# Kernel optimization log

Hardware: AMD Instinct MI355X
Metric: run time of the kernel (lower is better)

Reference implementation:

```python
import jax, jax.numpy as jnp
import numpy as np

E, H, V, B, T = 512, 512, 32000, 64, 20


def setup_inputs() -> dict:
    key = jax.random.key(0)
    ks = jax.random.split(key, 10)
    s = 0.05
    return {
        "features": jax.random.normal(ks[0], (B, E), jnp.float32),
        "captions": jax.random.randint(ks[1], (B, T), 0, V),
        "lenghts": jax.random.randint(ks[2], (B,), 1, T),
        "emb_table": jax.random.normal(ks[3], (V, E), jnp.float32) * s,
        "w_ih": jax.random.normal(ks[4], (4 * H, E), jnp.float32) * s,
        "w_hh": jax.random.normal(ks[5], (4 * H, H), jnp.float32) * s,
        "b_ih": jax.random.normal(ks[6], (4 * H,), jnp.float32) * s,
        "b_hh": jax.random.normal(ks[7], (4 * H,), jnp.float32) * s,
        "fc_w": jax.random.normal(ks[8], (V, H), jnp.float32) * s,
        "fc_b": jax.random.normal(ks[9], (V,), jnp.float32) * s,
    }


def _lstm(xs, w_ih, w_hh, b_ih, b_hh):
    # xs: [B, T+1, E] -> hidden states [B, T+1, H], PyTorch gate order i,f,g,o
    b, _, _ = xs.shape
    h0 = jnp.zeros((b, w_hh.shape[1]), xs.dtype)
    c0 = jnp.zeros_like(h0)
    bias = b_ih + b_hh

    def step(carry, x_t):
        h, c = carry
        gates = x_t @ w_ih.T + h @ w_hh.T + bias  # [B, 4H]
        i, f, g, o = jnp.split(gates, 4, axis=-1)
        i, f, o = jax.nn.sigmoid(i), jax.nn.sigmoid(f), jax.nn.sigmoid(o)
        g = jnp.tanh(g)
        c = f * c + i * g
        h = o * jnp.tanh(c)
        return (h, c), h

    _, hs = jax.lax.scan(step, (h0, c0), jnp.swapaxes(xs, 0, 1))  # hs: [T+1, B, H]
    return jnp.swapaxes(hs, 0, 1)


def reference(features, captions, lenghts, emb_table, w_ih, w_hh, b_ih, b_hh, fc_w, fc_b):
    embeddings = emb_table[captions]                       # [B, T, E]
    xs = jnp.concatenate([features[:, None, :], embeddings], axis=1)  # [B, T+1, E]
    hs = _lstm(xs, w_ih, w_hh, b_ih, b_hh)[:, 1:, :]       # [B, T, H]
    logits = hs @ fc_w.T + fc_b                            # [B, T, V]
    # original loops softmax over each 1-D vocab slice == softmax over last axis
    return jax.nn.softmax(logits, axis=-1)
```

## Files before the change

kernel.cpp:

```cpp
#include <hip/hip_runtime.h>
#include <cstdint>
#include <cstddef>

#define E_DIM 512
#define H_DIM 512
#define V_DIM 32000
#define B_DIM 64
#define T_DIM 20
#define NBLK 32
#define NBLK_TOT 256
#define PT_LDS 68
#define HS_STR 532

typedef _Float16 f16;
typedef _Float16 f16x8 __attribute__((ext_vector_type(8)));
typedef _Float16 f16x4 __attribute__((ext_vector_type(4)));
typedef float    f32x4 __attribute__((ext_vector_type(4)));

__device__ __forceinline__ void async_lds16(void* lds, const void* g) {
  __builtin_amdgcn_global_load_lds(
      (const __attribute__((address_space(1))) uint32_t*)g,
      (__attribute__((address_space(3))) uint32_t*)lds, 16, 0, 0);
}

__device__ __forceinline__ float sigmoidf_(float x) {
  return 1.0f / (1.0f + expf(-x));
}

__device__ __forceinline__ f16x8 load_h8_coh(const f16* p) {
  union { unsigned long long u[2]; f16x8 v; } r;
  r.u[0] = __hip_atomic_load((const unsigned long long*)p,
                             __ATOMIC_RELAXED, __HIP_MEMORY_SCOPE_AGENT);
  r.u[1] = __hip_atomic_load((const unsigned long long*)(p + 4),
                             __ATOMIC_RELAXED, __HIP_MEMORY_SCOPE_AGENT);
  return r.v;
}
__device__ __forceinline__ void store_h4_coh(f16* p, f16x4 v) {
  union { f16x4 h; unsigned long long u; } cvt;
  cvt.h = v;
  __hip_atomic_store((unsigned long long*)p, cvt.u,
                     __ATOMIC_RELAXED, __HIP_MEMORY_SCOPE_AGENT);
}

__global__ __launch_bounds__(128) void gather_x16_kernel(
    const float* __restrict__ features, const int* __restrict__ captions,
    const float* __restrict__ emb, f16* __restrict__ x16) {
  const int m = blockIdx.x;
  const int j = threadIdx.x;
  f16x4 r4 = {(f16)0.f, (f16)0.f, (f16)0.f, (f16)0.f};
  if (m < 1344) {
    const int b = m & 63;
    const int t = m >> 6;
    const float* src = (t == 0)
        ? features + (size_t)b * E_DIM
        : emb + (size_t)captions[b * T_DIM + (t - 1)] * E_DIM;
    const float4 v = ((const float4*)src)[j];
    r4.x = (f16)v.x; r4.y = (f16)v.y; r4.z = (f16)v.z; r4.w = (f16)v.w;
  }
  ((f16x4*)(x16 + (size_t)m * 512))[j] = r4;
}

__global__ __launch_bounds__(256) void convert_w_kernel(
    const float* __restrict__ w, f16* __restrict__ w16) {
  const int i = blockIdx.x * 256 + threadIdx.x;
  const float4 v = ((const float4*)w)[i];
  f16x4 r;
  r.x = (f16)v.x; r.y = (f16)v.y; r.z = (f16)v.z; r.w = (f16)v.w;
  ((f16x4*)w16)[i] = r;
}

__global__ __launch_bounds__(256) void bias_sum_kernel(
    const float* __restrict__ a, const float* __restrict__ b,
    float* __restrict__ o) {
  const int i = blockIdx.x * 256 + threadIdx.x;
  if (i < 2048) o[i] = a[i] + b[i];
}

__global__ __launch_bounds__(256) void gemm16_kernel(
    const f16* __restrict__ A, const f16* __restrict__ Bw,
    const float* __restrict__ bias, float* __restrict__ C, int ldc,
    int mode) {
  __shared__ f16 As[128 * 64];
  __shared__ f16 Bs[128 * 64];
  const int tid = threadIdx.x;
  const int lane = tid & 63;
  const int wid = tid >> 6;
  const int m0 = blockIdx.y * 128;
  const int n0 = blockIdx.x * 128;
  const int wm = (wid >> 1) * 64;
  const int wn = (wid & 1) * 64;

  f32x4 acc[4][4];
#pragma unroll
  for (int i = 0; i < 4; ++i)
#pragma unroll
    for (int j = 0; j < 4; ++j) {
      f32x4 z = {0.f, 0.f, 0.f, 0.f};
      acc[i][j] = z;
    }
  const int lr = lane & 15;
  const int lkb = (lane >> 4) * 8;

  for (int kt = 0; kt < 512; kt += 64) {
#pragma unroll
    for (int i = 0; i < 4; ++i) {
      const int off = i * 4096 + wid * 1024 + lane * 16;
      const int row = off >> 7;
      const int colh = (off & 127) >> 1;
      async_lds16((char*)As + i * 4096 + wid * 1024,
                  A + (size_t)(m0 + row) * 512 + kt + colh);
      async_lds16((char*)Bs + i * 4096 + wid * 1024,
                  Bw + (size_t)(n0 + row) * 512 + kt + colh);
    }
    __syncthreads();
#pragma unroll
    for (int ks = 0; ks < 2; ++ks) {
      f16x8 af[4], bf[4];
#pragma unroll
      for (int mi = 0; mi < 4; ++mi)
        af[mi] = *(const f16x8*)&As[(wm + mi * 16 + lr) * 64 + ks * 32 + lkb];
#pragma unroll
      for (int ni = 0; ni < 4; ++ni)
        bf[ni] = *(const f16x8*)&Bs[(wn + ni * 16 + lr) * 64 + ks * 32 + lkb];
#pragma unroll
      for (int mi = 0; mi < 4; ++mi)
#pragma unroll
        for (int ni = 0; ni < 4; ++ni)
          acc[mi][ni] = __builtin_amdgcn_mfma_f32_16x16x32_f16(
              af[mi], bf[ni], acc[mi][ni], 0, 0, 0);
    }
    __syncthreads();
  }

#pragma unroll
  for (int mi = 0; mi < 4; ++mi) {
    const int mbase = m0 + wm + mi * 16 + (lane >> 4) * 4;
#pragma unroll
    for (int ni = 0; ni < 4; ++ni) {
      const int n = n0 + wn + ni * 16 + lr;
      const float bv = bias[n];
#pragma unroll
      for (int r = 0; r < 4; ++r) {
        const int mr = mbase + r;
        size_t off;
        if (mode == 2)
          off = (size_t)(mr >> 6) * (2048 * 64) + (size_t)n * 64 + (mr & 63);
        else if (mode == 1)
          off = (size_t)((mr & 63) * 20 + (mr >> 6)) * ldc + n;
        else
          off = (size_t)mr * ldc + n;
        C[off] = acc[mi][ni][r] + bv;
      }
    }
  }
}

__global__ __launch_bounds__(256) void gemm16_f16out_kernel(
    const f16* __restrict__ A, const f16* __restrict__ Bw,
    const float* __restrict__ bias, f16* __restrict__ C16) {
  __shared__ f16 As[128 * 64];
  __shared__ f16 Bs[128 * 64];
  const int tid = threadIdx.x;
  const int lane = tid & 63;
  const int wid = tid >> 6;
  const int m0 = blockIdx.y * 128;
  const int n0 = blockIdx.x * 128;
  const int wm = (wid >> 1) * 64;
  const int wn = (wid & 1) * 64;

  f32x4 acc[4][4];
#pragma unroll
  for (int i = 0; i < 4; ++i)
#pragma unroll
    for (int j = 0; j < 4; ++j) {
      f32x4 z = {0.f, 0.f, 0.f, 0.f};
      acc[i][j] = z;
    }
  const int lr = lane & 15;
  const int lkb = (lane >> 4) * 8;

  for (int kt = 0; kt < 512; kt += 64) {
#pragma unroll
    for (int i = 0; i < 4; ++i) {
      const int off = i * 4096 + wid * 1024 + lane * 16;
      const int row = off >> 7;
      const int colh = (off & 127) >> 1;
      async_lds16((char*)As + i * 4096 + wid * 1024,
                  A + (size_t)(m0 + row) * 512 + kt + colh);
      async_lds16((char*)Bs + i * 4096 + wid * 1024,
                  Bw + (size_t)(n0 + row) * 512 + kt + colh);
    }
    __syncthreads();
#pragma unroll
    for (int ks = 0; ks < 2; ++ks) {
      f16x8 af[4], bf[4];
#pragma unroll
      for (int mi = 0; mi < 4; ++mi)
        af[mi] = *(const f16x8*)&As[(wm + mi * 16 + lr) * 64 + ks * 32 + lkb];
#pragma unroll
      for (int ni = 0; ni < 4; ++ni)
        bf[ni] = *(const f16x8*)&Bs[(wn + ni * 16 + lr) * 64 + ks * 32 + lkb];
#pragma unroll
      for (int mi = 0; mi < 4; ++mi)
#pragma unroll
        for (int ni = 0; ni < 4; ++ni)
          acc[mi][ni] = __builtin_amdgcn_mfma_f32_16x16x32_f16(
              af[mi], bf[ni], acc[mi][ni], 0, 0, 0);
    }
    __syncthreads();
  }

#pragma unroll
  for (int mi = 0; mi < 4; ++mi) {
    const int mbase = m0 + wm + mi * 16 + (lane >> 4) * 4;
#pragma unroll
    for (int ni = 0; ni < 4; ++ni) {
      const int n = n0 + wn + ni * 16 + lr;
      const float bv = bias[n];
#pragma unroll
      for (int r = 0; r < 4; ++r) {
        const int mr = mbase + r;
        const int orow = (mr & 63) * 20 + (mr >> 6);
        C16[(size_t)orow * 32000 + n] = (f16)(acc[mi][ni][r] + bv);
      }
    }
  }
}

__global__ __launch_bounds__(256, 1) void lstm_persistent7(
    const float* __restrict__ PT, const f16* __restrict__ Whh,
    f16* __restrict__ hsT, unsigned* __restrict__ flags,
    const float* __restrict__ fcw, f16* __restrict__ w16) {
  __shared__ f16 hS[64 * HS_STR];
  __shared__ float pT[64 * PT_LDS];
  __shared__ f16 hS2[64 * 16];
  const int tid = threadIdx.x;

  if (blockIdx.x >= NBLK) {
    const int g0 = (blockIdx.x - NBLK) * 256 + tid;
    for (int i = g0; i < 4096000; i += (NBLK_TOT - NBLK) * 256) {
      const float4 v = ((const float4*)fcw)[i];
      f16x4 r;
      r.x = (f16)v.x; r.y = (f16)v.y; r.z = (f16)v.z; r.w = (f16)v.w;
      ((f16x4*)w16)[i] = r;
    }
    return;
  }

  const int lane = tid & 63;
  const int w = tid >> 6;
  const int u0 = blockIdx.x * 16;
  const int fr = lane & 15;
  const int fq = lane >> 4;
  const int q = fr >> 2;
  const int jw = fr & 3;
  const int grow = q * 512 + u0 + w * 4 + jw;

  f16x8 bW[16];
  {
    const f16* brow = Whh + (size_t)grow * 512;
#pragma unroll
    for (int kk = 0; kk < 16; ++kk)
      bW[kk] = *(const f16x8*)&brow[kk * 32 + fq * 8];
  }

  for (int i = tid; i < 64 * 16; i += 256) {
    const int rr = i >> 4;
    const int q4 = i & 15;
    const int g = rr >> 4, ul = rr & 15;
    const float4 v =
        *(const float4*)&PT[((size_t)(g * 512 + u0 + ul)) * 64 + q4 * 4];
    *(float4*)&pT[rr * PT_LDS + q4 * 4] = v;
  }

  float cr[4] = {0.f, 0.f, 0.f, 0.f};

  for (int t = 0; t <= T_DIM; ++t) {
    if (t > 0) {
      const f16* src = hsT + (size_t)(t - 1) * (64 * 512)
                           + (size_t)(w * 16) * 512;
      f16x8 hrow[16];
#pragma unroll
      for (int j = 0; j < 16; ++j)
        hrow[j] = load_h8_coh(src + (size_t)j * 512 + lane * 8);
#pragma unroll
      for (int j = 0; j < 16; ++j)
        *(f16x8*)&hS[(w * 16 + j) * HS_STR + lane * 8] = hrow[j];
    }
    __syncthreads();

    f32x4 acc[4];
#pragma unroll
    for (int mi = 0; mi < 4; ++mi) {
      f32x4 z = {0.f, 0.f, 0.f, 0.f};
      acc[mi] = z;
    }
    if (t > 0) {
#pragma unroll
      for (int mi = 0; mi < 4; ++mi) {
        f16x8 a[16];
#pragma unroll
        for (int kk = 0; kk < 16; ++kk)
          a[kk] =
              *(const f16x8*)&hS[(mi * 16 + fr) * HS_STR + kk * 32 + fq * 8];
#pragma unroll
        for (int kk = 0; kk < 16; ++kk)
          acc[mi] = __builtin_amdgcn_mfma_f32_16x16x32_f16(a[kk], bW[kk],
                                                           acc[mi], 0, 0, 0);
      }
    }
    const int prow = (q * 16 + w * 4 + jw) * PT_LDS;
#pragma unroll
    for (int mi = 0; mi < 4; ++mi)
#pragma unroll
      for (int r = 0; r < 4; ++r)
        acc[mi][r] += pT[prow + mi * 16 + fq * 4 + r];

#pragma unroll
    for (int r = 0; r < 4; ++r) {
      const float y0 = acc[0][r], y1 = acc[1][r], y2 = acc[2][r],
                  y3 = acc[3][r];
      const float f0 = __shfl_xor(y0, 4),  f1 = __shfl_xor(y1, 4),
                  f2 = __shfl_xor(y2, 4),  f3 = __shfl_xor(y3, 4);
      const float g0 = __shfl_xor(y0, 8),  g1 = __shfl_xor(y1, 8),
                  g2 = __shfl_xor(y2, 8),  g3 = __shfl_xor(y3, 8);
      const float o0 = __shfl_xor(y0, 12), o1 = __shfl_xor(y1, 12),
                  o2 = __shfl_xor(y2, 12), o3 = __shfl_xor(y3, 12);
      const float x  = q == 0 ? y0 : q == 1 ? y1 : q == 2 ? y2 : y3;
      const float xf = q == 0 ? f0 : q == 1 ? f1 : q == 2 ? f2 : f3;
      const float xg = q == 0 ? g0 : q == 1 ? g1 : q == 2 ? g2 : g3;
      const float xo = q == 0 ? o0 : q == 1 ? o1 : q == 2 ? o2 : o3;
      const float gi = q == 0 ? x  : q == 1 ? xf : q == 2 ? xg : xo;
      const float gf = q == 0 ? xf : q == 1 ? x  : q == 2 ? xo : xg;
      const float gg = q == 0 ? xg : q == 1 ? xo : q == 2 ? x  : xf;
      const float go = q == 0 ? xo : q == 1 ? xg : q == 2 ? xf : x;
      const float si = sigmoidf_(gi);
      const float sf = sigmoidf_(gf);
      const float tg = tanhf(gg);
      const float so = sigmoidf_(go);
      const float cn = sf * cr[r] + si * tg;
      cr[r] = cn;
      const float hn = so * tanhf(cn);
      const int b = q * 16 + fq * 4 + r;
      hS2[b * 16 + w * 4 + jw] = (f16)hn;
    }
    __syncthreads();

    {
      f16* slab = hsT + (size_t)t * (64 * 512);
      const int row = tid >> 2;
      const int c4 = tid & 3;
      const f16x4 v = *(const f16x4*)&hS2[row * 16 + c4 * 4];
      store_h4_coh(slab + (size_t)row * 512 + u0 + c4 * 4, v);
    }

    if (t < T_DIM) {
      for (int i = tid; i < 64 * 16; i += 256) {
        const int rr = i >> 4;
        const int q4 = i & 15;
        const int g = rr >> 4, ul = rr & 15;
        const float4 v = *(const float4*)
            &PT[((size_t)(t + 1) * 2048 + g * 512 + u0 + ul) * 64 + q4 * 4];
        *(float4*)&pT[rr * PT_LDS + q4 * 4] = v;
      }
      asm volatile("s_waitcnt vmcnt(0)" ::: "memory");
      __syncthreads();
      if (tid == 0)
        __hip_atomic_store(&flags[blockIdx.x * 16], (unsigned)(t + 1),
                           __ATOMIC_RELAXED, __HIP_MEMORY_SCOPE_AGENT);
      if (tid < NBLK) {
        while (__hip_atomic_load(&flags[tid * 16], __ATOMIC_RELAXED,
                                 __HIP_MEMORY_SCOPE_AGENT) < (unsigned)(t + 1))
          __builtin_amdgcn_s_sleep(3);
      }
      __syncthreads();
    }
  }
}

__device__ __forceinline__ float waveMax(float v) {
#pragma unroll
  for (int o = 32; o > 0; o >>= 1) v = fmaxf(v, __shfl_down(v, o));
  return v;
}
__device__ __forceinline__ float waveSum(float v) {
#pragma unroll
  for (int o = 32; o > 0; o >>= 1) v += __shfl_down(v, o);
  return v;
}

__global__ __launch_bounds__(1024) void softmax_f16_kernel(
    const f16* __restrict__ lg, float* __restrict__ out) {
  const f16x8* L = (const f16x8*)(lg + (size_t)blockIdx.x * V_DIM);
  float4* p4 = (float4*)(out + (size_t)blockIdx.x * V_DIM);
  const int t = threadIdx.x;
  __shared__ float sred[16];

  float4 v[8];
  float m = -1e30f;
#pragma unroll
  for (int j = 0; j < 4; ++j) {
    const int i = j * 1024 + t;
    if (i < 4000) {
      const f16x8 h = L[i];
      v[2 * j].x     = (float)h[0]; v[2 * j].y     = (float)h[1];
      v[2 * j].z     = (float)h[2]; v[2 * j].w     = (float)h[3];
      v[2 * j + 1].x = (float)h[4]; v[2 * j + 1].y = (float)h[5];
      v[2 * j + 1].z = (float)h[6]; v[2 * j + 1].w = (float)h[7];
      m = fmaxf(m, fmaxf(fmaxf(v[2 * j].x, v[2 * j].y),
                         fmaxf(v[2 * j].z, v[2 * j].w)));
      m = fmaxf(m, fmaxf(fmaxf(v[2 * j + 1].x, v[2 * j + 1].y),
                         fmaxf(v[2 * j + 1].z, v[2 * j + 1].w)));
    }
  }
  m = waveMax(m);
  if ((t & 63) == 0) sred[t >> 6] = m;
  __syncthreads();
  float mb = sred[0];
#pragma unroll
  for (int k = 1; k < 16; ++k) mb = fmaxf(mb, sred[k]);
  __syncthreads();

  float s = 0.f;
#pragma unroll
  for (int j = 0; j < 8; ++j) {
    const int i = (j >> 1) * 1024 + t;
    if (i < 4000) {
      v[j].x = expf(v[j].x - mb);
      v[j].y = expf(v[j].y - mb);
      v[j].z = expf(v[j].z - mb);
      v[j].w = expf(v[j].w - mb);
      s += v[j].x + v[j].y + v[j].z + v[j].w;
    }
  }
  s = waveSum(s);
  if ((t & 63) == 0) sred[t >> 6] = s;
  __syncthreads();
  float sb = sred[0];
#pragma unroll
  for (int k = 1; k < 16; ++k) sb += sred[k];
  const float inv = 1.0f / sb;

#pragma unroll
  for (int j = 0; j < 4; ++j) {
    const int i = j * 1024 + t;
    if (i < 4000) {
      float4 a = v[2 * j], b = v[2 * j + 1];
      a.x *= inv; a.y *= inv; a.z *= inv; a.w *= inv;
      b.x *= inv; b.y *= inv; b.z *= inv; b.w *= inv;
      p4[2 * i] = a;
      p4[2 * i + 1] = b;
    }
  }
}

__global__ __launch_bounds__(1024) void softmax_reg_kernel(
    float* __restrict__ out) {
  float4* p4 = (float4*)(out + (size_t)blockIdx.x * V_DIM);
  const int t = threadIdx.x;
  __shared__ float sred[16];
  float4 v[8];
  float m = -1e30f;
#pragma unroll
  for (int j = 0; j < 8; ++j) {
    const int i = j * 1024 + t;
    if (i < 8000) {
      v[j] = p4[i];
      m = fmaxf(m, fmaxf(fmaxf(v[j].x, v[j].y), fmaxf(v[j].z, v[j].w)));
    }
  }
  m = waveMax(m);
  if ((t & 63) == 0) sred[t >> 6] = m;
  __syncthreads();
  float mb = sred[0];
#pragma unroll
  for (int k = 1; k < 16; ++k) mb = fmaxf(mb, sred[k]);
  __syncthreads();
  float s = 0.f;
#pragma unroll
  for (int j = 0; j < 8; ++j) {
    const int i = j * 1024 + t;
    if (i < 8000) {
      v[j].x = expf(v[j].x - mb);
      v[j].y = expf(v[j].y - mb);
      v[j].z = expf(v[j].z - mb);
      v[j].w = expf(v[j].w - mb);
      s += v[j].x + v[j].y + v[j].z + v[j].w;
    }
  }
  s = waveSum(s);
  if ((t & 63) == 0) sred[t >> 6] = s;
  __syncthreads();
  float sb = sred[0];
#pragma unroll
  for (int k = 1; k < 16; ++k) sb += sred[k];
  const float inv = 1.0f / sb;
#pragma unroll
  for (int j = 0; j < 8; ++j) {
    const int i = j * 1024 + t;
    if (i < 8000) {
      float4 o;
      o.x = v[j].x * inv; o.y = v[j].y * inv;
      o.z = v[j].z * inv; o.w = v[j].w * inv;
      p4[i] = o;
    }
  }
}

extern "C" void kernel_launch(void* const* d_in, const int* in_sizes, int n_in,
                              void* d_out, int out_size, void* d_ws, size_t ws_size,
                              hipStream_t stream) {
  const float* features = (const float*)d_in[0];
  const int*   captions = (const int*)d_in[1];
  const float* emb      = (const float*)d_in[3];
  const float* w_ih     = (const float*)d_in[4];
  const float* w_hh     = (const float*)d_in[5];
  const float* b_ih     = (const float*)d_in[6];
  const float* b_hh     = (const float*)d_in[7];
  const float* fc_w     = (const float*)d_in[8];
  const float* fc_b     = (const float*)d_in[9];
  float* out = (float*)d_out;

  char* ws = (char*)d_ws;
  unsigned* flags = (unsigned*)ws; ws += 2048;
  f16* hsT = (f16*)ws;  ws += (size_t)21 * B_DIM * H_DIM * 2;
  f16* w16 = (f16*)ws;  ws += (size_t)V_DIM * H_DIM * 2;
  f16* logits16 = (f16*)ws;
  const size_t ws_need_f16logits =
      ((char*)logits16 - (char*)d_ws) + (size_t)1280 * V_DIM * 2;
  const bool use_f16_logits = ws_size >= ws_need_f16logits;

  float* PT    = out;
  f16*   x16   = (f16*)(out + 3000000);
  f16*   wih16 = (f16*)(out + 3400000);
  f16*   whh16 = (f16*)(out + 4000000);
  float* bsum  = out + 4600000;

  hipMemsetAsync(flags, 0, 2048, stream);

  gather_x16_kernel<<<1408, 128, 0, stream>>>(features, captions, emb, x16);
  convert_w_kernel<<<1024, 256, 0, stream>>>(w_ih, wih16);
  convert_w_kernel<<<1024, 256, 0, stream>>>(w_hh, whh16);
  bias_sum_kernel<<<8, 256, 0, stream>>>(b_ih, b_hh, bsum);

  gemm16_kernel<<<dim3(16, 11), 256, 0, stream>>>(x16, wih16, bsum, PT, 0, 2);

  lstm_persistent7<<<NBLK_TOT, 256, 0, stream>>>(PT, whh16, hsT, flags,
                                                 fc_w, w16);

  const f16* Afc = hsT + (size_t)B_DIM * H_DIM;
  if (use_f16_logits) {
    gemm16_f16out_kernel<<<dim3(250, 10), 256, 0, stream>>>(Afc, w16, fc_b,
                                                            logits16);
    softmax_f16_kernel<<<1280, 1024, 0, stream>>>(logits16, out);
  } else {
    gemm16_kernel<<<dim3(250, 10), 256, 0, stream>>>(Afc, w16, fc_b, out,
                                                     32000, 1);
    softmax_reg_kernel<<<1280, 1024, 0, stream>>>(out);
  }
}
```

Baseline: 308.2 us.

## Fuse FC GEMM into persistent LSTM kernel with dynamic tile queue and per-timestep flags

Merges the output-projection GEMM into the persistent LSTM kernel. After the recurrence (or the fc_w conversion), blocks pull 128x128 tiles from an atomic queue. Each tile waits only on the LSTM flags for the timesteps it needs, so FC work on early timesteps can overlap the remaining recurrence and one kernel launch disappears. The cost is spin-waiting and a non-async, coherent load path for the A operand. The GEMM also runs on only 256 blocks at one block per CU, fewer than the original 2500-block grid.

Result: slower. 372.1 us (+20.7%).

```diff
diff --git a/kernel.cpp b/kernel.cpp
--- a/kernel.cpp
+++ b/kernel.cpp
@@ -11,6 +11,7 @@
 #define NBLK_TOT 256
 #define PT_LDS 68
 #define HS_STR 532
+#define N_TILES 2500
 
 typedef _Float16 f16;
 typedef _Float16 f16x8 __attribute__((ext_vector_type(8)));
@@ -155,86 +156,20 @@
   }
 }
 
-__global__ __launch_bounds__(256) void gemm16_f16out_kernel(
-    const f16* __restrict__ A, const f16* __restrict__ Bw,
-    const float* __restrict__ bias, f16* __restrict__ C16) {
-  __shared__ f16 As[128 * 64];
-  __shared__ f16 Bs[128 * 64];
-  const int tid = threadIdx.x;
-  const int lane = tid & 63;
-  const int wid = tid >> 6;
-  const int m0 = blockIdx.y * 128;
-  const int n0 = blockIdx.x * 128;
-  const int wm = (wid >> 1) * 64;
-  const int wn = (wid & 1) * 64;
-
-  f32x4 acc[4][4];
-#pragma unroll
-  for (int i = 0; i < 4; ++i)
-#pragma unroll
-    for (int j = 0; j < 4; ++j) {
-      f32x4 z = {0.f, 0.f, 0.f, 0.f};
-      acc[i][j] = z;
-    }
-  const int lr = lane & 15;
-  const int lkb = (lane >> 4) * 8;
-
-  for (int kt = 0; kt < 512; kt += 64) {
-#pragma unroll
-    for (int i = 0; i < 4; ++i) {
-      const int off = i * 4096 + wid * 1024 + lane * 16;
-      const int row = off >> 7;
-      const int colh = (off & 127) >> 1;
-      async_lds16((char*)As + i * 4096 + wid * 1024,
-                  A + (size_t)(m0 + row) * 512 + kt + colh);
-      async_lds16((char*)Bs + i * 4096 + wid * 1024,
-                  Bw + (size_t)(n0 + row) * 512 + kt + colh);
-    }
-    __syncthreads();
-#pragma unroll
-    for (int ks = 0; ks < 2; ++ks) {
-      f16x8 af[4], bf[4];
-#pragma unroll
-      for (int mi = 0; mi < 4; ++mi)
-        af[mi] = *(const f16x8*)&As[(wm + mi * 16 + lr) * 64 + ks * 32 + lkb];
-#pragma unroll
-      for (int ni = 0; ni < 4; ++ni)
-        bf[ni] = *(const f16x8*)&Bs[(wn + ni * 16 + lr) * 64 + ks * 32 + lkb];
-#pragma unroll
-      for (int mi = 0; mi < 4; ++mi)
-#pragma unroll
-        for (int ni = 0; ni < 4; ++ni)
-          acc[mi][ni] = __builtin_amdgcn_mfma_f32_16x16x32_f16(
-              af[mi], bf[ni], acc[mi][ni], 0, 0, 0);
-    }
-    __syncthreads();
-  }
-
-#pragma unroll
-  for (int mi = 0; mi < 4; ++mi) {
-    const int mbase = m0 + wm + mi * 16 + (lane >> 4) * 4;
-#pragma unroll
-    for (int ni = 0; ni < 4; ++ni) {
-      const int n = n0 + wn + ni * 16 + lr;
-      const float bv = bias[n];
-#pragma unroll
-      for (int r = 0; r < 4; ++r) {
-        const int mr = mbase + r;
-        const int orow = (mr & 63) * 20 + (mr >> 6);
-        C16[(size_t)orow * 32000 + n] = (f16)(acc[mi][ni][r] + bv);
-      }
-    }
-  }
-}
-
-__global__ __launch_bounds__(256, 1) void lstm_persistent7(
+__global__ __launch_bounds__(256, 1) void mega_kernel(
     const float* __restrict__ PT, const f16* __restrict__ Whh,
     f16* __restrict__ hsT, unsigned* __restrict__ flags,
-    const float* __restrict__ fcw, f16* __restrict__ w16) {
+    const float* __restrict__ fcw, f16* __restrict__ w16,
+    const float* __restrict__ fcb, f16* __restrict__ logits16,
+    unsigned* __restrict__ convDone, unsigned* __restrict__ queue,
+    int do_fc) {
   __shared__ f16 hS[64 * HS_STR];
   __shared__ float pT[64 * PT_LDS];
   __shared__ f16 hS2[64 * 16];
+  __shared__ unsigned tileS;
   const int tid = threadIdx.x;
+  const int lane = tid & 63;
+  const int w = tid >> 6;
 
   if (blockIdx.x >= NBLK) {
     const int g0 = (blockIdx.x - NBLK) * 256 + tid;
@@ -242,138 +177,247 @@
       const float4 v = ((const float4*)fcw)[i];
       f16x4 r;
       r.x = (f16)v.x; r.y = (f16)v.y; r.z = (f16)v.z; r.w = (f16)v.w;
-      ((f16x4*)w16)[i] = r;
-    }
-    return;
-  }
-
-  const int lane = tid & 63;
-  const int w = tid >> 6;
-  const int u0 = blockIdx.x * 16;
-  const int fr = lane & 15;
-  const int fq = lane >> 4;
-  const int q = fr >> 2;
-  const int jw = fr & 3;
-  const int grow = q * 512 + u0 + w * 4 + jw;
-
-  f16x8 bW[16];
-  {
-    const f16* brow = Whh + (size_t)grow * 512;
-#pragma unroll
-    for (int kk = 0; kk < 16; ++kk)
-      bW[kk] = *(const f16x8*)&brow[kk * 32 + fq * 8];
-  }
-
-  for (int i = tid; i < 64 * 16; i += 256) {
-    const int rr = i >> 4;
-    const int q4 = i & 15;
-    const int g = rr >> 4, ul = rr & 15;
-    const float4 v =
-        *(const float4*)&PT[((size_t)(g * 512 + u0 + ul)) * 64 + q4 * 4];
-    *(float4*)&pT[rr * PT_LDS + q4 * 4] = v;
-  }
-
-  float cr[4] = {0.f, 0.f, 0.f, 0.f};
-
-  for (int t = 0; t <= T_DIM; ++t) {
-    if (t > 0) {
-      const f16* src = hsT + (size_t)(t - 1) * (64 * 512)
-                           + (size_t)(w * 16) * 512;
-      f16x8 hrow[16];
-#pragma unroll
-      for (int j = 0; j < 16; ++j)
-        hrow[j] = load_h8_coh(src + (size_t)j * 512 + lane * 8);
-#pragma unroll
-      for (int j = 0; j < 16; ++j)
-        *(f16x8*)&hS[(w * 16 + j) * HS_STR + lane * 8] = hrow[j];
-    }
+      store_h4_coh(w16 + (size_t)i * 4, r);
+    }
+    asm volatile("s_waitcnt vmcnt(0)" ::: "memory");
     __syncthreads();
-
-    f32x4 acc[4];
+    if (tid == 0)
+      __hip_atomic_fetch_add(convDone, 1u, __ATOMIC_RELAXED,
+                             __HIP_MEMORY_SCOPE_AGENT);
+  } else {
+    const int u0 = blockIdx.x * 16;
+    const int fr = lane & 15;
+    const int fq = lane >> 4;
+    const int q = fr >> 2;
+    const int jw = fr & 3;
+    const int grow = q * 512 + u0 + w * 4 + jw;
+
+    f16x8 bW[16];
+    {
+      const f16* brow = Whh + (size_t)grow * 512;
+#pragma unroll
+      for (int kk = 0; kk < 16; ++kk)
+        bW[kk] = *(const f16x8*)&brow[kk * 32 + fq * 8];
+    }
+    for (int i = tid; i < 64 * 16; i += 256) {
+      const int rr = i >> 4;
+      const int q4 = i & 15;
+      const int g = rr >> 4, ul = rr & 15;
+      const float4 v =
+          *(const float4*)&PT[((size_t)(g * 512 + u0 + ul)) * 64 + q4 * 4];
+      *(float4*)&pT[rr * PT_LDS + q4 * 4] = v;
+    }
+
+    float cr[4] = {0.f, 0.f, 0.f, 0.f};
+
+    for (int t = 0; t <= T_DIM; ++t) {
+      if (t > 0) {
+        const f16* src = hsT + (size_t)(t - 1) * (64 * 512)
+                             + (size_t)(w * 16) * 512;
+        f16x8 hrow[16];
+#pragma unroll
+        for (int j = 0; j < 16; ++j)
+          hrow[j] = load_h8_coh(src + (size_t)j * 512 + lane * 8);
+#pragma unroll
+        for (int j = 0; j < 16; ++j)
+          *(f16x8*)&hS[(w * 16 + j) * HS_STR + lane * 8] = hrow[j];
+      }
+      __syncthreads();
+
+      f32x4 acc[4];
+#pragma unroll
+      for (int mi = 0; mi < 4; ++mi) {
+        f32x4 z = {0.f, 0.f, 0.f, 0.f};
+        acc[mi] = z;
+      }
+      if (t > 0) {
+#pragma unroll
+        for (int mi = 0; mi < 4; ++mi) {
+          f16x8 a[16];
+#pragma unroll
+          for (int kk = 0; kk < 16; ++kk)
+            a[kk] =
+                *(const f16x8*)&hS[(mi * 16 + fr) * HS_STR + kk * 32 + fq * 8];
+#pragma unroll
+          for (int kk = 0; kk < 16; ++kk)
+            acc[mi] = __builtin_amdgcn_mfma_f32_16x16x32_f16(a[kk], bW[kk],
+                                                             acc[mi], 0, 0, 0);
+        }
+      }
+      const int prow = (q * 16 + w * 4 + jw) * PT_LDS;
+#pragma unroll
+      for (int mi = 0; mi < 4; ++mi)
+#pragma unroll
+        for (int r = 0; r < 4; ++r)
+          acc[mi][r] += pT[prow + mi * 16 + fq * 4 + r];
+
+#pragma unroll
+      for (int r = 0; r < 4; ++r) {
+        const float y0 = acc[0][r], y1 = acc[1][r], y2 = acc[2][r],
+                    y3 = acc[3][r];
+        const float f0 = __shfl_xor(y0, 4),  f1 = __shfl_xor(y1, 4),
+                    f2 = __shfl_xor(y2, 4),  f3 = __shfl_xor(y3, 4);
+        const float g0 = __shfl_xor(y0, 8),  g1 = __shfl_xor(y1, 8),
+                    g2 = __shfl_xor(y2, 8),  g3 = __shfl_xor(y3, 8);
+        const float o0 = __shfl_xor(y0, 12), o1 = __shfl_xor(y1, 12),
+                    o2 = __shfl_xor(y2, 12), o3 = __shfl_xor(y3, 12);
+        const float x  = q == 0 ? y0 : q == 1 ? y1 : q == 2 ? y2 : y3;
+        const float xf = q == 0 ? f0 : q == 1 ? f1 : q == 2 ? f2 : f3;
+        const float xg = q == 0 ? g0 : q == 1 ? g1 : q == 2 ? g2 : g3;
+        const float xo = q == 0 ? o0 : q == 1 ? o1 : q == 2 ? o2 : o3;
+        const float gi = q == 0 ? x  : q == 1 ? xf : q == 2 ? xg : xo;
+        const float gf = q == 0 ? xf : q == 1 ? x  : q == 2 ? xo : xg;
+        const float gg = q == 0 ? xg : q == 1 ? xo : q == 2 ? x  : xf;
+        const float go = q == 0 ? xo : q == 1 ? xg : q == 2 ? xf : x;
+        const float si = sigmoidf_(gi);
+        const float sf = sigmoidf_(gf);
+        const float tg = tanhf(gg);
+        const float so = sigmoidf_(go);
+        const float cn = sf * cr[r] + si * tg;
+        cr[r] = cn;
+        const float hn = so * tanhf(cn);
+        const int b = q * 16 + fq * 4 + r;
+        hS2[b * 16 + w * 4 + jw] = (f16)hn;
+      }
+      __syncthreads();
+      {
+        f16* slab = hsT + (size_t)t * (64 * 512);
+        const int row = tid >> 2;
+        const int c4 = tid & 3;
+        const f16x4 v = *(const f16x4*)&hS2[row * 16 + c4 * 4];
+        store_h4_coh(slab + (size_t)row * 512 + u0 + c4 * 4, v);
+      }
+
+      if (t < T_DIM) {
+        for (int i = tid; i < 64 * 16; i += 256) {
+          const int rr = i >> 4;
+          const int q4 = i & 15;
+          const int g = rr >> 4, ul = rr & 15;
+          const float4 v = *(const float4*)
+              &PT[((size_t)(t + 1) * 2048 + g * 512 + u0 + ul) * 64 + q4 * 4];
+          *(float4*)&pT[rr * PT_LDS + q4 * 4] = v;
+        }
+        asm volatile("s_waitcnt vmcnt(0)" ::: "memory");
+        __syncthreads();
+        if (tid == 0)
+          __hip_atomic_store(&flags[blockIdx.x * 16], (unsigned)(t + 1),
+                             __ATOMIC_RELAXED, __HIP_MEMORY_SCOPE_AGENT);
+        if (tid < NBLK) {
+          while (__hip_atomic_load(&flags[tid * 16], __ATOMIC_RELAXED,
+                                   __HIP_MEMORY_SCOPE_AGENT) <
+                 (unsigned)(t + 1))
+            __builtin_amdgcn_s_sleep(3);
+        }
+        __syncthreads();
+      }
+    }
+    asm volatile("s_waitcnt vmcnt(0)" ::: "memory");
+    __syncthreads();
+    if (tid == 0)
+      __hip_atomic_store(&flags[blockIdx.x * 16], (unsigned)(T_DIM + 1),
+                         __ATOMIC_RELAXED, __HIP_MEMORY_SCOPE_AGENT);
+  }
+
+  if (!do_fc) return;
+
+  if (tid == 0) {
+    while (__hip_atomic_load(convDone, __ATOMIC_RELAXED,
+                             __HIP_MEMORY_SCOPE_AGENT) <
+           (unsigned)(NBLK_TOT - NBLK))
+      __builtin_amdgcn_s_sleep(3);
+  }
+  __syncthreads();
+
+  const f16* Afc = hsT + (size_t)B_DIM * H_DIM;
+  f16* As = hS;
+  f16* Bs = hS + 128 * 64;
+  const int lr = lane & 15;
+  const int lkb = (lane >> 4) * 8;
+  const int wm = (w >> 1) * 64;
+  const int wn = (w & 1) * 64;
+
+  for (;;) {
+    if (tid == 0)
+      tileS = __hip_atomic_fetch_add(queue, 1u, __ATOMIC_RELAXED,
+                                     __HIP_MEMORY_SCOPE_AGENT);
+    __syncthreads();
+    const unsigned tile = tileS;
+    __syncthreads();
+    if (tile >= (unsigned)N_TILES) break;
+    const int mt = (int)tile / 250;
+    const int nt = (int)tile % 250;
+    const int m0 = mt * 128;
+    const int n0 = nt * 128;
+
+    if (tid < NBLK) {
+      const unsigned need = (unsigned)(3 + 2 * mt);
+      while (__hip_atomic_load(&flags[tid * 16], __ATOMIC_RELAXED,
+                               __HIP_MEMORY_SCOPE_AGENT) < need)
+        __builtin_amdgcn_s_sleep(3);
+    }
+    __syncthreads();
+
+    f32x4 acc[4][4];
+#pragma unroll
+    for (int i = 0; i < 4; ++i)
+#pragma unroll
+      for (int j = 0; j < 4; ++j) {
+        f32x4 z = {0.f, 0.f, 0.f, 0.f};
+        acc[i][j] = z;
+      }
+
+    for (int kt = 0; kt < 512; kt += 64) {
+      for (int i = tid; i < 1024; i += 256) {
+        const int row = i >> 3;
+        const int ch = i & 7;
+        const f16x8 v =
+            load_h8_coh(Afc + (size_t)(m0 + row) * 512 + kt + ch * 8);
+        *(f16x8*)&As[row * 64 + ch * 8] = v;
+      }
+#pragma unroll
+      for (int i = 0; i < 4; ++i) {
+        const int off = i * 4096 + w * 1024 + lane * 16;
+        const int row = off >> 7;
+        const int colh = (off & 127) >> 1;
+        async_lds16((char*)Bs + i * 4096 + w * 1024,
+                    w16 + (size_t)(n0 + row) * 512 + kt + colh);
+      }
+      __syncthreads();
+#pragma unroll
+      for (int ks = 0; ks < 2; ++ks) {
+        f16x8 af[4], bf[4];
+#pragma unroll
+        for (int mi = 0; mi < 4; ++mi)
+          af[mi] =
+              *(const f16x8*)&As[(wm + mi * 16 + lr) * 64 + ks * 32 + lkb];
+#pragma unroll
+        for (int ni = 0; ni < 4; ++ni)
+          bf[ni] =
+              *(const f16x8*)&Bs[(wn + ni * 16 + lr) * 64 + ks * 32 + lkb];
+#pragma unroll
+        for (int mi = 0; mi < 4; ++mi)
+#pragma unroll
+          for (int ni = 0; ni < 4; ++ni)
+            acc[mi][ni] = __builtin_amdgcn_mfma_f32_16x16x32_f16(
+                af[mi], bf[ni], acc[mi][ni], 0, 0, 0);
+      }
+      __syncthreads();
+    }
+
 #pragma unroll
     for (int mi = 0; mi < 4; ++mi) {
-      f32x4 z = {0.f, 0.f, 0.f, 0.f};
-      acc[mi] = z;
-    }
-    if (t > 0) {
-#pragma unroll
-      for (int mi = 0; mi < 4; ++mi) {
-        f16x8 a[16];
-#pragma unroll
-        for (int kk = 0; kk < 16; ++kk)
-          a[kk] =
-              *(const f16x8*)&hS[(mi * 16 + fr) * HS_STR + kk * 32 + fq * 8];
-#pragma unroll
-        for (int kk = 0; kk < 16; ++kk)
-          acc[mi] = __builtin_amdgcn_mfma_f32_16x16x32_f16(a[kk], bW[kk],
-                                                           acc[mi], 0, 0, 0);
-      }
-    }
-    const int prow = (q * 16 + w * 4 + jw) * PT_LDS;
-#pragma unroll
-    for (int mi = 0; mi < 4; ++mi)
-#pragma unroll
-      for (int r = 0; r < 4; ++r)
-        acc[mi][r] += pT[prow + mi * 16 + fq * 4 + r];
-
-#pragma unroll
-    for (int r = 0; r < 4; ++r) {
-      const float y0 = acc[0][r], y1 = acc[1][r], y2 = acc[2][r],
-                  y3 = acc[3][r];
-      const float f0 = __shfl_xor(y0, 4),  f1 = __shfl_xor(y1, 4),
-                  f2 = __shfl_xor(y2, 4),  f3 = __shfl_xor(y3, 4);
-      const float g0 = __shfl_xor(y0, 8),  g1 = __shfl_xor(y1, 8),
-                  g2 = __shfl_xor(y2, 8),  g3 = __shfl_xor(y3, 8);
-      const float o0 = __shfl_xor(y0, 12), o1 = __shfl_xor(y1, 12),
-                  o2 = __shfl_xor(y2, 12), o3 = __shfl_xor(y3, 12);
-      const float x  = q == 0 ? y0 : q == 1 ? y1 : q == 2 ? y2 : y3;
-      const float xf = q == 0 ? f0 : q == 1 ? f1 : q == 2 ? f2 : f3;
-      const float xg = q == 0 ? g0 : q == 1 ? g1 : q == 2 ? g2 : g3;
-      const float xo = q == 0 ? o0 : q == 1 ? o1 : q == 2 ? o2 : o3;
-      const float gi = q == 0 ? x  : q == 1 ? xf : q == 2 ? xg : xo;
-      const float gf = q == 0 ? xf : q == 1 ? x  : q == 2 ? xo : xg;
-      const float gg = q == 0 ? xg : q == 1 ? xo : q == 2 ? x  : xf;
-      const float go = q == 0 ? xo : q == 1 ? xg : q == 2 ? xf : x;
-      const float si = sigmoidf_(gi);
-      const float sf = sigmoidf_(gf);
-      const float tg = tanhf(gg);
-      const float so = sigmoidf_(go);
-      const float cn = sf * cr[r] + si * tg;
-      cr[r] = cn;
-      const float hn = so * tanhf(cn);
-      const int b = q * 16 + fq * 4 + r;
-      hS2[b * 16 + w * 4 + jw] = (f16)hn;
-    }
-    __syncthreads();
-
-    {
-      f16* slab = hsT + (size_t)t * (64 * 512);
-      const int row = tid >> 2;
-      const int c4 = tid & 3;
-      const f16x4 v = *(const f16x4*)&hS2[row * 16 + c4 * 4];
-      store_h4_coh(slab + (size_t)row * 512 + u0 + c4 * 4, v);
-    }
-
-    if (t < T_DIM) {
-      for (int i = tid; i < 64 * 16; i += 256) {
-        const int rr = i >> 4;
-        const int q4 = i & 15;
-        const int g = rr >> 4, ul = rr & 15;
-        const float4 v = *(const float4*)
-            &PT[((size_t)(t + 1) * 2048 + g * 512 + u0 + ul) * 64 + q4 * 4];
-        *(float4*)&pT[rr * PT_LDS + q4 * 4] = v;
-      }
-      asm volatile("s_waitcnt vmcnt(0)" ::: "memory");
-      __syncthreads();
-      if (tid == 0)
-        __hip_atomic_store(&flags[blockIdx.x * 16], (unsigned)(t + 1),
-                           __ATOMIC_RELAXED, __HIP_MEMORY_SCOPE_AGENT);
-      if (tid < NBLK) {
-        while (__hip_atomic_load(&flags[tid * 16], __ATOMIC_RELAXED,
-                                 __HIP_MEMORY_SCOPE_AGENT) < (unsigned)(t + 1))
-          __builtin_amdgcn_s_sleep(3);
-      }
-      __syncthreads();
+      const int mbase = m0 + wm + mi * 16 + (lane >> 4) * 4;
+#pragma unroll
+      for (int ni = 0; ni < 4; ++ni) {
+        const int n = n0 + wn + ni * 16 + lr;
+        const float bv = fcb[n];
+#pragma unroll
+        for (int r = 0; r < 4; ++r) {
+          const int mr = mbase + r;
+          const int orow = (mr & 63) * 20 + (mr >> 6);
+          logits16[(size_t)orow * 32000 + n] = (f16)(acc[mi][ni][r] + bv);
+        }
+      }
     }
   }
 }
@@ -522,7 +566,9 @@
   float* out = (float*)d_out;
 
   char* ws = (char*)d_ws;
-  unsigned* flags = (unsigned*)ws; ws += 2048;
+  unsigned* flags = (unsigned*)ws; ws += 4096;
+  unsigned* convDone = flags + 512;
+  unsigned* queue    = flags + 528;
   f16* hsT = (f16*)ws;  ws += (size_t)21 * B_DIM * H_DIM * 2;
   f16* w16 = (f16*)ws;  ws += (size_t)V_DIM * H_DIM * 2;
   f16* logits16 = (f16*)ws;
@@ -536,7 +582,7 @@
   f16*   whh16 = (f16*)(out + 4000000);
   float* bsum  = out + 4600000;
 
-  hipMemsetAsync(flags, 0, 2048, stream);
+  hipMemsetAsync(flags, 0, 4096, stream);
 
   gather_x16_kernel<<<1408, 128, 0, stream>>>(features, captions, emb, x16);
   convert_w_kernel<<<1024, 256, 0, stream>>>(w_ih, wih16);
@@ -545,15 +591,14 @@
 
   gemm16_kernel<<<dim3(16, 11), 256, 0, stream>>>(x16, wih16, bsum, PT, 0, 2);
 
-  lstm_persistent7<<<NBLK_TOT, 256, 0, stream>>>(PT, whh16, hsT, flags,
-                                                 fc_w, w16);
-
-  const f16* Afc = hsT + (size_t)B_DIM * H_DIM;
+  mega_kernel<<<NBLK_TOT, 256, 0, stream>>>(PT, whh16, hsT, flags, fc_w, w16,
+                                            fc_b, logits16, convDone, queue,
+                                            use_f16_logits ? 1 : 0);
+
   if (use_f16_logits) {
-    gemm16_f16out_kernel<<<dim3(250, 10), 256, 0, stream>>>(Afc, w16, fc_b,
-                                                            logits16);
     softmax_f16_kernel<<<1280, 1024, 0, stream>>>(logits16, out);
   } else {
+    const f16* Afc = hsT + (size_t)B_DIM * H_DIM;
     gemm16_kernel<<<dim3(250, 10), 256, 0, stream>>>(Afc, w16, fc_b, out,
                                                      32000, 1);
     softmax_reg_kernel<<<1280, 1024, 0, stream>>>(out);
```
